# Kernel optimization log

Measured on AMD Instinct MI355X. Metric: run time of the kernel, lower is better.

Reference implementation:

```python
import jax, jax.numpy as jnp
import numpy as np

BETA = 0.95
THR = 1.0
SLOPE = 25.0


@jax.custom_vjp
def spike(x):
    # heaviside(x) with fast_sigmoid surrogate gradient (slope=25)
    return (x > 0).astype(x.dtype)

def _spike_fwd(x):
    return (x > 0).astype(x.dtype), x

def _spike_bwd(x, g):
    return (g / (SLOPE * jnp.abs(x) + 1.0) ** 2,)

spike.defvjp(_spike_fwd, _spike_bwd)


def setup_inputs() -> dict:
    key = jax.random.key(0)
    ks = jax.random.split(key, 16)
    T, B, D_in, H, C = 25, 128, 2048, 4096, 1000
    P_ACTIVE = 0.1

    def sparse_layer(kw, kb, km, fan_in, fan_out):
        bound = (6.0 / fan_in) ** 0.5  # kaiming_uniform with a=sqrt(5) -> U(-sqrt(6/fan_in)*?, ...); approx scale
        w = jax.random.uniform(kw, (fan_out, fan_in), minval=-bound, maxval=bound, dtype=jnp.float32)
        mask = (jax.random.uniform(km, (fan_out, fan_in)) < P_ACTIVE).astype(jnp.float32)
        # rescale rows by sqrt(fan_in / fan_in_active) on active weights
        fan_act = jnp.clip(mask.sum(axis=1, keepdims=True), 1.0, None)
        scale = jnp.where((fan_act > 0) & (fan_act < fan_in), (fan_in / fan_act) ** 0.5, 1.0)
        w = jnp.where(mask > 0, w * scale, w)
        fan_eff = jnp.maximum(mask.sum(axis=1).mean(), 1.0)
        b_bound = 1.0 / fan_eff ** 0.5
        b = jax.random.uniform(kb, (fan_out,), minval=-b_bound, maxval=b_bound, dtype=jnp.float32)
        return w, b, mask

    w1, b1, m1 = sparse_layer(ks[0], ks[1], ks[2], D_in, H)
    w2, b2, m2 = sparse_layer(ks[3], ks[4], ks[5], H, H)
    w3, b3, m3 = sparse_layer(ks[6], ks[7], ks[8], H, H)
    bo_bound = 1.0 / H ** 0.5
    w_out = jax.random.uniform(ks[9], (C, H), minval=-bo_bound, maxval=bo_bound, dtype=jnp.float32)
    b_out = jax.random.uniform(ks[10], (C,), minval=-bo_bound, maxval=bo_bound, dtype=jnp.float32)
    x_seq = jax.random.normal(ks[11], (T, B, D_in), dtype=jnp.float32)
    return {"x_seq": x_seq, "w1": w1, "b1": b1, "m1": m1, "w2": w2, "b2": b2, "m2": m2,
            "w3": w3, "b3": b3, "m3": m3, "w_out": w_out, "b_out": b_out}


def _lif(cur, mem):
    # snntorch Leaky, reset_mechanism='subtract': reset spike from PREVIOUS mem, detached
    reset = jax.lax.stop_gradient((mem > THR).astype(mem.dtype))
    mem_new = BETA * mem + cur - reset * THR
    spk = spike(mem_new - THR)
    return spk, mem_new


def reference(x_seq, w1, b1, m1, w2, b2, m2, w3, b3, m3, w_out, b_out):
    T, B, _ = x_seq.shape
    ew1 = w1 * m1  # effective weights cached once (math identical to per-step recompute)
    ew2 = w2 * m2
    ew3 = w3 * m3

    mem1 = jnp.zeros((B, ew1.shape[0]), x_seq.dtype)
    mem2 = jnp.zeros((B, ew2.shape[0]), x_seq.dtype)
    mem3 = jnp.zeros((B, ew3.shape[0]), x_seq.dtype)
    mem_o = jnp.zeros((B, w_out.shape[0]), x_seq.dtype)
    spk_sum = jnp.zeros((B, w_out.shape[0]), x_seq.dtype)

    def step(carry, x_t):
        mem1, mem2, mem3, mem_o, spk_sum = carry
        spk1, mem1 = _lif(x_t @ ew1.T + b1, mem1)
        spk2, mem2 = _lif(spk1 @ ew2.T + b2, mem2)
        spk3, mem3 = _lif(spk2 @ ew3.T + b3, mem3)
        spk_o, mem_o = _lif(spk3 @ w_out.T + b_out, mem_o)
        return (mem1, mem2, mem3, mem_o, spk_sum + spk_o), None

    (mem1, mem2, mem3, mem_o, spk_sum), _ = jax.lax.scan(
        step, (mem1, mem2, mem3, mem_o, spk_sum), x_seq)
    return spk_sum
```

## Files before the change

### kernel.cpp

```cpp
#include <hip/hip_runtime.h>

#define T_STEPS 25
#define BATCH   128
#define D_IN    2048
#define H_DIM   4096
#define C_DIM   1000
#define N_ALL   3200
#define GEMM_Q  320
#define P_K2048 7
#define P_K4096 13
#define WOT_LD  1024

typedef __attribute__((address_space(1))) const void gas_t;
typedef __attribute__((address_space(3))) void las_t;

__device__ __forceinline__ int panel_len(int rem) {
    return (rem >= 2 * GEMM_Q) ? GEMM_Q
         : (rem > GEMM_Q ? ((rem / 2 + 15) & ~15) : rem);
}

__global__ __launch_bounds__(256)
void tmask_k(float* __restrict__ dst, const float* __restrict__ src,
             const float* __restrict__ msk, int M, int K, int MT)
{
    __shared__ float t[32][33];
    const int tx = threadIdx.x, ty = threadIdx.y;
    const int k0 = blockIdx.x * 32, m0 = blockIdx.y * 32;
    #pragma unroll
    for (int i = 0; i < 4; ++i) {
        const int m = m0 + ty + 8 * i;
        float v = 0.f;
        if (m < M) {
            const size_t gi = (size_t)m * K + k0 + tx;
            v = src[gi];
            if (msk) v *= msk[gi];
        }
        t[ty + 8 * i][tx] = v;
    }
    __syncthreads();
    const int mc = m0 + tx;
    if (mc < MT) {
        #pragma unroll
        for (int i = 0; i < 4; ++i)
            dst[(size_t)(k0 + ty + 8 * i) * MT + mc] = t[tx][ty + 8 * i];
    }
}

#define FMAQ(AS, R)                                                   \
    acc[R].x = fmaf(AS, bv.x, acc[R].x);                              \
    acc[R].y = fmaf(AS, bv.y, acc[R].y);                              \
    acc[R].z = fmaf(AS, bv.z, acc[R].z);                              \
    acc[R].w = fmaf(AS, bv.w, acc[R].w);

__global__ __launch_bounds__(256)
void gemm_w(const float* __restrict__ AT, const float* __restrict__ B,
            float* __restrict__ part, int MT, int K, int ldb, int n0)
{
#pragma clang fp reassociate(off)
    __shared__ __align__(16) float Bs[2][16][128];
    __shared__ __align__(16) float As[4][2][16][16];
    const int tid  = threadIdx.x;
    const int w    = tid >> 6;
    const int lane = tid & 63;
    const int mg   = lane >> 5;
    const int lc   = lane & 31;
    const int m0   = blockIdx.y * 64 + w * 16;
    const int p    = blockIdx.x;

    int pstart = 0, rem = K, pl = panel_len(K);
    for (int i = 0; i < p; ++i) { pstart += pl; rem -= pl; pl = panel_len(rem); }
    const int nt = pl >> 4;

    float4 acc[8];
    #pragma unroll
    for (int r = 0; r < 8; ++r) acc[r] = make_float4(0.f, 0.f, 0.f, 0.f);

    const int akr = lane >> 2, amq = (lane & 3) * 4;
    const float* ap = AT + (size_t)(pstart + akr) * MT + m0 + amq;
    const float* bsrc = B + (size_t)(pstart + w * 4 + (lane >> 5)) * ldb + n0 + lc * 4;

    {
        __builtin_amdgcn_global_load_lds((gas_t*)ap, (las_t*)&As[w][0][0][0], 16, 0, 0);
        __builtin_amdgcn_global_load_lds((gas_t*)bsrc,
                                         (las_t*)&Bs[0][w * 4][0], 16, 0, 0);
        __builtin_amdgcn_global_load_lds((gas_t*)(bsrc + 2 * (size_t)ldb),
                                         (las_t*)&Bs[0][w * 4 + 2][0], 16, 0, 0);
    }
    __syncthreads();

    for (int ti = 0; ti < nt; ++ti) {
        const int bf = ti & 1;
        if (ti + 1 < nt) {
            const float* a2 = ap + (size_t)(ti + 1) * 16 * MT;
            const float* b2 = bsrc + (size_t)(ti + 1) * 16 * ldb;
            __builtin_amdgcn_global_load_lds((gas_t*)a2, (las_t*)&As[w][bf ^ 1][0][0], 16, 0, 0);
            __builtin_amdgcn_global_load_lds((gas_t*)b2,
                                             (las_t*)&Bs[bf ^ 1][w * 4][0], 16, 0, 0);
            __builtin_amdgcn_global_load_lds((gas_t*)(b2 + 2 * (size_t)ldb),
                                             (las_t*)&Bs[bf ^ 1][w * 4 + 2][0], 16, 0, 0);
        }
        #pragma unroll
        for (int kk = 0; kk < 16; ++kk) {
            const float4 a0 = *(const float4*)&As[w][bf][kk][mg * 8];
            const float4 a1 = *(const float4*)&As[w][bf][kk][mg * 8 + 4];
            const float4 bv = *(const float4*)&Bs[bf][kk][lc * 4];
            FMAQ(a0.x, 0) FMAQ(a0.y, 1) FMAQ(a0.z, 2) FMAQ(a0.w, 3)
            FMAQ(a1.x, 4) FMAQ(a1.y, 5) FMAQ(a1.z, 6) FMAQ(a1.w, 7)
        }
        __syncthreads();
    }

    const int mrow0 = m0 + mg * 8;
    #pragma unroll
    for (int r = 0; r < 8; ++r)
        *(float4*)&part[((size_t)p * MT + mrow0 + r) * BATCH + lc * 4] = acc[r];
}

__device__ __forceinline__ float lif1e(float c, float& m)
{
    const float r = (m > 1.0f) ? 1.0f : 0.0f;
    const float mn = __fsub_rn(__fadd_rn(__fmul_rn(0.95f, m), c), r);
    m = mn;
    return (mn > 1.0f) ? 1.0f : 0.0f;
}

__global__ __launch_bounds__(256)
void reduce_lif4(const float* __restrict__ part, int P, int Mdim,
                 const float* __restrict__ bias, float* __restrict__ mem,
                 float* __restrict__ spk)
{
#pragma clang fp reassociate(off)
    const int idx4 = blockIdx.x * 256 + threadIdx.x;
    const int idx = idx4 * 4;
    const size_t stride = (size_t)Mdim * BATCH;
    float4 tot = *(const float4*)&part[idx];
    for (int z = 1; z < P; ++z) {
        const float4 pv = *(const float4*)&part[(size_t)z * stride + idx];
        tot.x = __fadd_rn(tot.x, pv.x); tot.y = __fadd_rn(tot.y, pv.y);
        tot.z = __fadd_rn(tot.z, pv.z); tot.w = __fadd_rn(tot.w, pv.w);
    }
    const float bb = bias[idx >> 7];
    float4 mm = *(float4*)&mem[idx];
    float4 sp;
    sp.x = lif1e(__fadd_rn(tot.x, bb), mm.x);
    sp.y = lif1e(__fadd_rn(tot.y, bb), mm.y);
    sp.z = lif1e(__fadd_rn(tot.z, bb), mm.z);
    sp.w = lif1e(__fadd_rn(tot.w, bb), mm.w);
    *(float4*)&mem[idx] = mm;
    *(float4*)&spk[idx] = sp;
}

__global__ __launch_bounds__(256)
void reduce_lif_out4(const float* __restrict__ part, int P, int Mpad,
                     const float* __restrict__ bias, float* __restrict__ mem,
                     float* __restrict__ out)
{
#pragma clang fp reassociate(off)
    const int idx4 = blockIdx.x * 256 + threadIdx.x;
    if (idx4 >= (C_DIM * BATCH) / 4) return;
    const int idx = idx4 * 4;
    const int cc = idx >> 7, b = idx & 127;
    const size_t stride = (size_t)Mpad * BATCH;
    float4 tot = *(const float4*)&part[idx];
    for (int z = 1; z < P; ++z) {
        const float4 pv = *(const float4*)&part[(size_t)z * stride + idx];
        tot.x = __fadd_rn(tot.x, pv.x); tot.y = __fadd_rn(tot.y, pv.y);
        tot.z = __fadd_rn(tot.z, pv.z); tot.w = __fadd_rn(tot.w, pv.w);
    }
    const float bb = bias[cc];
    float4 mm = *(float4*)&mem[idx];
    float s;
    s = lif1e(__fadd_rn(tot.x, bb), mm.x); if (s > 0.f) out[(size_t)(b+0) * C_DIM + cc] += 1.0f;
    s = lif1e(__fadd_rn(tot.y, bb), mm.y); if (s > 0.f) out[(size_t)(b+1) * C_DIM + cc] += 1.0f;
    s = lif1e(__fadd_rn(tot.z, bb), mm.z); if (s > 0.f) out[(size_t)(b+2) * C_DIM + cc] += 1.0f;
    s = lif1e(__fadd_rn(tot.w, bb), mm.w); if (s > 0.f) out[(size_t)(b+3) * C_DIM + cc] += 1.0f;
    *(float4*)&mem[idx] = mm;
}

extern "C" void kernel_launch(void* const* d_in, const int* in_sizes, int n_in,
                              void* d_out, int out_size, void* d_ws, size_t ws_size,
                              hipStream_t stream)
{
    const float* x  = (const float*)d_in[0];
    const float* w1 = (const float*)d_in[1];
    const float* b1 = (const float*)d_in[2];
    const float* m1 = (const float*)d_in[3];
    const float* w2 = (const float*)d_in[4];
    const float* b2 = (const float*)d_in[5];
    const float* m2 = (const float*)d_in[6];
    const float* w3 = (const float*)d_in[7];
    const float* b3 = (const float*)d_in[8];
    const float* m3 = (const float*)d_in[9];
    const float* wo = (const float*)d_in[10];
    const float* bo = (const float*)d_in[11];
    float* out = (float*)d_out;
    float* ws  = (float*)d_ws;
    (void)in_sizes; (void)n_in; (void)ws_size;

    const size_t HB = (size_t)H_DIM * BATCH;
    const size_t CB = (size_t)C_DIM * BATCH;

    size_t off = 0;
    const size_t MEM1 = off; off += HB;
    const size_t MEM2 = off; off += HB;
    const size_t MEM3 = off; off += HB;
    const size_t MEMO = off; off += CB;
    const size_t stateFloats = off;
    const size_t SPK1 = off; off += HB;
    const size_t SPK2 = off; off += HB;
    const size_t SPK3 = off; off += HB;
    const size_t PART = off; off += (size_t)P_K4096 * HB;
    const size_t EWT1 = off; off += (size_t)D_IN * H_DIM;
    const size_t EWT2 = off; off += (size_t)H_DIM * H_DIM;
    const size_t EWT3 = off; off += (size_t)H_DIM * H_DIM;
    const size_t WOT  = off; off += (size_t)H_DIM * WOT_LD;
    const size_t XT   = off; off += (size_t)D_IN * N_ALL;

    hipMemsetAsync(d_ws, 0, stateFloats * sizeof(float), stream);
    hipMemsetAsync(d_out, 0, (size_t)out_size * sizeof(float), stream);

    {
        dim3 tb(32, 8);
        tmask_k<<<dim3(D_IN / 32, H_DIM / 32), tb, 0, stream>>>(ws + EWT1, w1, m1, H_DIM, D_IN, H_DIM);
        tmask_k<<<dim3(H_DIM / 32, H_DIM / 32), tb, 0, stream>>>(ws + EWT2, w2, m2, H_DIM, H_DIM, H_DIM);
        tmask_k<<<dim3(H_DIM / 32, H_DIM / 32), tb, 0, stream>>>(ws + EWT3, w3, m3, H_DIM, H_DIM, H_DIM);
        tmask_k<<<dim3(H_DIM / 32, WOT_LD / 32), tb, 0, stream>>>(ws + WOT, wo, nullptr, C_DIM, H_DIM, WOT_LD);
        tmask_k<<<dim3(D_IN / 32, N_ALL / 32), tb, 0, stream>>>(ws + XT, x, nullptr, N_ALL, D_IN, N_ALL);
    }

    const dim3 g1(P_K2048, H_DIM / 64);
    const dim3 g23(P_K4096, H_DIM / 64);
    const dim3 go(P_K4096, WOT_LD / 64);
    const int gLif4  = (int)(HB / 4 / 256);
    const int gLifO4 = (int)((CB / 4 + 255) / 256);

    for (int t = 0; t < T_STEPS; ++t) {
        gemm_w<<<g1, 256, 0, stream>>>(ws + EWT1, ws + XT, ws + PART,
                                       H_DIM, D_IN, N_ALL, t * BATCH);
        reduce_lif4<<<gLif4, 256, 0, stream>>>(ws + PART, P_K2048, H_DIM, b1, ws + MEM1, ws + SPK1);

        gemm_w<<<g23, 256, 0, stream>>>(ws + EWT2, ws + SPK1, ws + PART,
                                        H_DIM, H_DIM, BATCH, 0);
        reduce_lif4<<<gLif4, 256, 0, stream>>>(ws + PART, P_K4096, H_DIM, b2, ws + MEM2, ws + SPK2);

        gemm_w<<<g23, 256, 0, stream>>>(ws + EWT3, ws + SPK2, ws + PART,
                                        H_DIM, H_DIM, BATCH, 0);
        reduce_lif4<<<gLif4, 256, 0, stream>>>(ws + PART, P_K4096, H_DIM, b3, ws + MEM3, ws + SPK3);

        gemm_w<<<go, 256, 0, stream>>>(ws + WOT, ws + SPK3, ws + PART,
                                       WOT_LD, H_DIM, BATCH, 0);
        reduce_lif_out4<<<gLifO4, 256, 0, stream>>>(ws + PART, P_K4096, WOT_LD, bo, ws + MEMO, out);
    }
}
```

Measured before the change: 5.195 ms.

## Read A operand via wave-uniform global loads instead of LDS staging

Drops the shared-memory staging buffer for the transposed A operand in the weight GEMM. Each wave now reads its 16 A rows directly from global memory with wave-uniform addresses, which the compiler can turn into scalar loads. The per-thread tile changes from 8x4 to 16x2 accumulators. This cuts LDS reads and the A prefetch path, but the A loads are no longer double-buffered, so global or scalar load latency may now sit in the inner loop.

```diff
diff --git a/kernel.cpp b/kernel.cpp
--- a/kernel.cpp
+++ b/kernel.cpp
@@ -46,24 +46,15 @@
     }
 }
 
-#define FMAQ(AS, R)                                                   \
-    acc[R].x = fmaf(AS, bv.x, acc[R].x);                              \
-    acc[R].y = fmaf(AS, bv.y, acc[R].y);                              \
-    acc[R].z = fmaf(AS, bv.z, acc[R].z);                              \
-    acc[R].w = fmaf(AS, bv.w, acc[R].w);
-
 __global__ __launch_bounds__(256)
 void gemm_w(const float* __restrict__ AT, const float* __restrict__ B,
             float* __restrict__ part, int MT, int K, int ldb, int n0)
 {
 #pragma clang fp reassociate(off)
     __shared__ __align__(16) float Bs[2][16][128];
-    __shared__ __align__(16) float As[4][2][16][16];
     const int tid  = threadIdx.x;
     const int w    = tid >> 6;
     const int lane = tid & 63;
-    const int mg   = lane >> 5;
-    const int lc   = lane & 31;
     const int m0   = blockIdx.y * 64 + w * 16;
     const int p    = blockIdx.x;
 
@@ -71,16 +62,14 @@
     for (int i = 0; i < p; ++i) { pstart += pl; rem -= pl; pl = panel_len(rem); }
     const int nt = pl >> 4;
 
-    float4 acc[8];
+    float2 acc[16];
     #pragma unroll
-    for (int r = 0; r < 8; ++r) acc[r] = make_float4(0.f, 0.f, 0.f, 0.f);
-
-    const int akr = lane >> 2, amq = (lane & 3) * 4;
-    const float* ap = AT + (size_t)(pstart + akr) * MT + m0 + amq;
-    const float* bsrc = B + (size_t)(pstart + w * 4 + (lane >> 5)) * ldb + n0 + lc * 4;
+    for (int r = 0; r < 16; ++r) acc[r] = make_float2(0.f, 0.f);
+
+    const float* bsrc = B + (size_t)(pstart + w * 4 + (lane >> 5)) * ldb + n0 + (lane & 31) * 4;
+    const float* abase = AT + (size_t)pstart * MT + m0;
 
     {
-        __builtin_amdgcn_global_load_lds((gas_t*)ap, (las_t*)&As[w][0][0][0], 16, 0, 0);
         __builtin_amdgcn_global_load_lds((gas_t*)bsrc,
                                          (las_t*)&Bs[0][w * 4][0], 16, 0, 0);
         __builtin_amdgcn_global_load_lds((gas_t*)(bsrc + 2 * (size_t)ldb),
@@ -91,29 +80,30 @@
     for (int ti = 0; ti < nt; ++ti) {
         const int bf = ti & 1;
         if (ti + 1 < nt) {
-            const float* a2 = ap + (size_t)(ti + 1) * 16 * MT;
             const float* b2 = bsrc + (size_t)(ti + 1) * 16 * ldb;
-            __builtin_amdgcn_global_load_lds((gas_t*)a2, (las_t*)&As[w][bf ^ 1][0][0], 16, 0, 0);
             __builtin_amdgcn_global_load_lds((gas_t*)b2,
                                              (las_t*)&Bs[bf ^ 1][w * 4][0], 16, 0, 0);
             __builtin_amdgcn_global_load_lds((gas_t*)(b2 + 2 * (size_t)ldb),
                                              (las_t*)&Bs[bf ^ 1][w * 4 + 2][0], 16, 0, 0);
         }
+        const float* atile = abase + (size_t)ti * 16 * MT;
         #pragma unroll
         for (int kk = 0; kk < 16; ++kk) {
-            const float4 a0 = *(const float4*)&As[w][bf][kk][mg * 8];
-            const float4 a1 = *(const float4*)&As[w][bf][kk][mg * 8 + 4];
-            const float4 bv = *(const float4*)&Bs[bf][kk][lc * 4];
-            FMAQ(a0.x, 0) FMAQ(a0.y, 1) FMAQ(a0.z, 2) FMAQ(a0.w, 3)
-            FMAQ(a1.x, 4) FMAQ(a1.y, 5) FMAQ(a1.z, 6) FMAQ(a1.w, 7)
+            const float* ar = atile + (size_t)kk * MT;
+            const float2 bv = *(const float2*)&Bs[bf][kk][lane * 2];
+            #pragma unroll
+            for (int r = 0; r < 16; ++r) {
+                const float av = ar[r];
+                acc[r].x = fmaf(av, bv.x, acc[r].x);
+                acc[r].y = fmaf(av, bv.y, acc[r].y);
+            }
         }
         __syncthreads();
     }
 
-    const int mrow0 = m0 + mg * 8;
     #pragma unroll
-    for (int r = 0; r < 8; ++r)
-        *(float4*)&part[((size_t)p * MT + mrow0 + r) * BATCH + lc * 4] = acc[r];
+    for (int r = 0; r < 16; ++r)
+        *(float2*)&part[((size_t)p * MT + m0 + r) * BATCH + lane * 2] = acc[r];
 }
 
 __device__ __forceinline__ float lif1e(float c, float& m)
```

After: 13.00 ms. 150% more time.
